# Performance work log

Hardware: AMD Instinct MI355X
Metric: run time of the kernel (lower is better)

The kernel has to match this reference:

```python
import jax, jax.numpy as jnp
import numpy as np

N, E, F_IN, D, H = 20000, 640000, 128, 16, 8  # nodes, edges, in_features, out_features, n_heads


def _linear_params(k, fan_in, fan_out):
    W = jax.random.normal(k, (fan_in, fan_out), jnp.float32) / np.sqrt(fan_in)
    b = jnp.zeros((fan_out,), jnp.float32)
    return W, b


def setup_inputs() -> dict:
    key = jax.random.key(0)
    ks = jax.random.split(key, 8)
    x = jax.random.normal(ks[0], (N, F_IN), jnp.float32)
    edge_index = jax.random.randint(ks[1], (2, E), 0, N, dtype=jnp.int64)
    Wq, bq = _linear_params(ks[2], F_IN, D * H)
    Wk, bk = _linear_params(ks[3], F_IN, D * H)
    Wv, bv = _linear_params(ks[4], F_IN, D * H)
    Wpsi, bpsi = _linear_params(ks[5], D, D)
    Wo, bo = _linear_params(ks[6], D * H * 2, F_IN)
    gamma = jnp.ones((F_IN,), jnp.float32)
    beta = jnp.zeros((F_IN,), jnp.float32)
    return {"x": x, "edge_index": edge_index, "Wq": Wq, "bq": bq, "Wk": Wk, "bk": bk,
            "Wv": Wv, "bv": bv, "Wpsi": Wpsi, "bpsi": bpsi, "Wo": Wo, "bo": bo,
            "gamma": gamma, "beta": beta}


def _segment_softmax(logits, seg, num_segments):
    # numerically-stable softmax of edge logits grouped by destination node (row)
    m = jax.ops.segment_max(logits, seg, num_segments=num_segments)  # [N,H]
    m = jnp.where(jnp.isfinite(m), m, 0.0)
    e = jnp.exp(logits - m[seg])  # [E,H]
    s = jax.ops.segment_sum(e, seg, num_segments=num_segments)  # [N,H]
    return e / (s[seg] + 1e-16)


def reference(x, edge_index, Wq, bq, Wk, bk, Wv, bv, Wpsi, bpsi, Wo, bo, gamma, beta):
    q = (x @ Wq + bq).reshape(N, H, D)
    k = (x @ Wk + bk).reshape(N, H, D)
    v = (x @ Wv + bv).reshape(N, H, D)
    row, col = edge_index[0], edge_index[1]

    logits = jnp.einsum('ehd,ehd->eh', q[row], k[col]) / np.sqrt(D)  # [E,H]
    alpha = _segment_softmax(logits, row, N)  # [E,H]

    v_j = v[col]  # [E,H,D]
    h_lp = jax.ops.segment_sum((alpha[..., None] * v_j).reshape(E, H * D), row, num_segments=N)
    v_bp = jnp.tanh(v_j @ Wpsi + bpsi)  # per-head linear on last dim, [E,H,D]
    h_bp = jax.ops.segment_sum((alpha[..., None] * v_bp).reshape(E, H * D), row, num_segments=N)

    h_out = jnp.concatenate([h_lp, h_bp], axis=1) @ Wo + bo  # [N,F_IN]
    y = x + jax.nn.relu(h_out)
    mu = jnp.mean(y, axis=-1, keepdims=True)
    var = jnp.mean(jnp.square(y - mu), axis=-1, keepdims=True)
    return (y - mu) * jax.lax.rsqrt(var + 1e-5) * gamma + beta
```

## Files before the change

### kernel.cpp

```cpp
#include <hip/hip_runtime.h>
#include <hip/hip_bf16.h>
#include <math.h>

#define NN 20000
#define EE 640000

typedef __attribute__((ext_vector_type(8))) short short8;
typedef __attribute__((ext_vector_type(4))) float f32x4;
typedef __hip_bfloat16 bf16;

__device__ inline ushort f2bf(float f) {
  bf16 h = __float2bfloat16(f);
  return *(ushort*)&h;
}
__device__ inline float bflo(uint u) { return __uint_as_float(u << 16); }
__device__ inline float bfhi(uint u) { return __uint_as_float(u & 0xFFFF0000u); }

__global__ __launch_bounds__(256) void prep_kernel(
    const float* __restrict__ x,
    const float* __restrict__ Wq, const float* __restrict__ Wk,
    const float* __restrict__ Wv, const float* __restrict__ Wo,
    const float* __restrict__ Wpsi, const float* __restrict__ bpsi,
    const float* __restrict__ bv,
    ushort* __restrict__ xb, ushort* __restrict__ Wts ,
    ushort* __restrict__ Wot, float* __restrict__ bvpsi) {
  __shared__ float T[128][129];
  __shared__ float WpsiS[256];
  __shared__ float bpsiS[16];
  int b = blockIdx.x, t = threadIdx.x;

  if (b < 1250) {
    int idx = b * 2048 + t * 8;
    const float* src = x + idx;
    float4 f0 = *(const float4*)(src);
    float4 f1 = *(const float4*)(src + 4);
    ushort tmp[8] = {f2bf(f0.x), f2bf(f0.y), f2bf(f0.z), f2bf(f0.w),
                     f2bf(f1.x), f2bf(f1.y), f2bf(f1.z), f2bf(f1.w)};
    *(uint4*)(xb + idx) = *(uint4*)tmp;
    return;
  }

  if (b <= 1254) {
    int which = b - 1250;
    const float* W;
    int k0 = 0;
    if (which < 3) W = (which == 0) ? Wq : (which == 1 ? Wk : Wv);
    else { W = Wo; k0 = (which - 3) * 128; }
    {
      int r = t >> 1, c0 = (t & 1) * 64;
      const float* src = W + (size_t)(k0 + r) * 128 + c0;
#pragma unroll
      for (int j = 0; j < 16; ++j) {
        float4 f = *(const float4*)(src + 4 * j);
        T[r][c0 + 4 * j + 0] = f.x; T[r][c0 + 4 * j + 1] = f.y;
        T[r][c0 + 4 * j + 2] = f.z; T[r][c0 + 4 * j + 3] = f.w;
      }
    }
    __syncthreads();
    int n = t >> 1, kh = (t & 1) * 64;
    if (which < 3) {
      ushort* dst = Wts + which * 16384 + n * 128 + kh;
#pragma unroll
      for (int j8 = 0; j8 < 8; ++j8) {
        ushort buf[8];
#pragma unroll
        for (int j = 0; j < 8; ++j) buf[j] = f2bf(T[kh + j8 * 8 + j][n]);
        *(uint4*)(dst + j8 * 8) = *(uint4*)buf;
      }
    } else {
      ushort* dst = Wot + n * 256 + k0 + kh;
#pragma unroll
      for (int j8 = 0; j8 < 8; ++j8) {
        ushort buf[8];
#pragma unroll
        for (int j = 0; j < 8; ++j) buf[j] = f2bf(T[kh + j8 * 8 + j][n]);
        *(uint4*)(dst + j8 * 8) = *(uint4*)buf;
      }
    }
    return;
  }

  {
    int r = t >> 1, c0 = (t & 1) * 64;
    const float* src = Wv + (size_t)r * 128 + c0;
#pragma unroll
    for (int j = 0; j < 16; ++j) {
      float4 f = *(const float4*)(src + 4 * j);
      T[r][c0 + 4 * j + 0] = f.x; T[r][c0 + 4 * j + 1] = f.y;
      T[r][c0 + 4 * j + 2] = f.z; T[r][c0 + 4 * j + 3] = f.w;
    }
    WpsiS[t] = Wpsi[t];
    if (t < 16) bpsiS[t] = bpsi[t];
  }
  __syncthreads();
  {
    int n = t >> 1, kh = (t & 1) * 64;
    int h = n >> 4, d = n & 15;
    ushort* dst = Wts + 3 * 16384 + n * 128 + kh;
    for (int k = 0; k < 64; ++k) {
      float acc = 0.f;
#pragma unroll
      for (int dp = 0; dp < 16; ++dp)
        acc = fmaf(T[kh + k][h * 16 + dp], WpsiS[dp * 16 + d], acc);
      dst[k] = f2bf(acc);
    }
    if (t < 128) {
      int hh = t >> 4, dd = t & 15;
      float acc = bpsiS[dd];
#pragma unroll
      for (int dp = 0; dp < 16; ++dp)
        acc = fmaf(bv[hh * 16 + dp], WpsiS[dp * 16 + dd], acc);
      bvpsi[t] = acc;
    }
  }
}

__global__ __launch_bounds__(256) void qkv_mfma(
    const ushort* __restrict__ xb, const ushort* __restrict__ Wts,
    const float* __restrict__ bq, const float* __restrict__ bk,
    const float* __restrict__ bv, const float* __restrict__ bvpsi,
    float* __restrict__ qbuf, ushort* __restrict__ kvb) {
  int t = threadIdx.x;
  int w = t >> 6, lane = t & 63;
  int m = lane & 15, qd = lane >> 4;
  int n0 = blockIdx.x * 128;
  int mat = blockIdx.y;
  const ushort* Wt = Wts + mat * 16384;
  const float* bias = (mat == 0) ? bq : (mat == 1 ? bk : (mat == 2 ? bv : bvpsi));
  int gr0 = n0 + w * 32;

  f32x4 acc0[8], acc1[8];
#pragma unroll
  for (int c = 0; c < 8; ++c) {
    acc0[c] = (f32x4){0.f, 0.f, 0.f, 0.f};
    acc1[c] = (f32x4){0.f, 0.f, 0.f, 0.f};
  }
#pragma unroll
  for (int kb = 0; kb < 4; ++kb) {
    int ko = kb * 32 + qd * 8;
    short8 a0 = *(const short8*)(xb + (size_t)(gr0 + m) * 128 + ko);
    short8 a1 = *(const short8*)(xb + (size_t)(gr0 + 16 + m) * 128 + ko);
#pragma unroll
    for (int c = 0; c < 8; ++c) {
      short8 bfr = *(const short8*)(Wt + (size_t)(c * 16 + m) * 128 + ko);
      acc0[c] = __builtin_amdgcn_mfma_f32_16x16x32_bf16(a0, bfr, acc0[c], 0, 0, 0);
      acc1[c] = __builtin_amdgcn_mfma_f32_16x16x32_bf16(a1, bfr, acc1[c], 0, 0, 0);
    }
  }
#pragma unroll
  for (int c = 0; c < 8; ++c) {
    int col = c * 16 + m;
    float bb = bias[col];
#pragma unroll
    for (int reg = 0; reg < 4; ++reg) {
      int row0 = gr0 + 4 * qd + reg;
      int row1 = row0 + 16;
      float v0 = acc0[c][reg] + bb;
      float v1 = acc1[c][reg] + bb;
      if (mat == 0) {
        if (row0 < NN) qbuf[(size_t)row0 * 128 + col] = v0;
        if (row1 < NN) qbuf[(size_t)row1 * 128 + col] = v1;
      } else if (mat < 3) {
        int off = (mat == 1) ? 0 : 128;
        if (row0 < NN) kvb[(size_t)row0 * 384 + off + col] = f2bf(v0);
        if (row1 < NN) kvb[(size_t)row1 * 384 + off + col] = f2bf(v1);
      } else {
        if (row0 < NN) kvb[(size_t)row0 * 384 + 256 + col] = f2bf(tanhf(v0));
        if (row1 < NN) kvb[(size_t)row1 * 384 + 256 + col] = f2bf(tanhf(v1));
      }
    }
  }
}

__global__ __launch_bounds__(256) void scatter_pad(const int* __restrict__ ei,
                                                   int* __restrict__ cursor,
                                                   int* __restrict__ scol) {
  int e = blockIdx.x * 256 + threadIdx.x;
  if (e < EE) {
    int r = ei[e];
    int c = ei[EE + e];
    int pos = atomicAdd(&cursor[r], 1);
    if (pos < 128) scol[r * 128 + pos] = c;
  }
}

__global__ __launch_bounds__(256) void aggregate_kernel(
    const float* __restrict__ qbuf, const ushort* __restrict__ kvb,
    const int* __restrict__ cursor, const int* __restrict__ scol,
    ushort* __restrict__ hb) {
  int wid = threadIdx.x >> 6, lane = threadIdx.x & 63;
  int node = blockIdx.x * 4 + wid;
  int e = lane >> 3, h = lane & 7;
  const float SC = 0.25f * 1.44269504f;

  float qv[16];
  {
    const float* qp = qbuf + (size_t)node * 128 + h * 16;
#pragma unroll
    for (int j = 0; j < 4; ++j) {
      float4 f = *(const float4*)(qp + 4 * j);
      qv[4 * j + 0] = f.x * SC; qv[4 * j + 1] = f.y * SC;
      qv[4 * j + 2] = f.z * SC; qv[4 * j + 3] = f.w * SC;
    }
  }
  int cnt = cursor[node];
  cnt = cnt > 128 ? 128 : cnt;
  int base = node * 128;

  float s = 0.f;
  float accV[16], accB[16];
#pragma unroll
  for (int j = 0; j < 16; ++j) { accV[j] = 0.f; accB[j] = 0.f; }

  for (int i0 = 0; i0 < cnt; i0 += 8) {
    int idx = i0 + e;
    bool valid = idx < cnt;
    int col = scol[base + (valid ? idx : 0)];
    const ushort* B = kvb + (size_t)col * 384 + h * 16;
    uint4 ka = *(const uint4*)(B);
    uint4 kb4 = *(const uint4*)(B + 8);
    uint4 va = *(const uint4*)(B + 128);
    uint4 vb4 = *(const uint4*)(B + 136);
    uint4 ta = *(const uint4*)(B + 256);
    uint4 tb4 = *(const uint4*)(B + 264);
    uint kk[8] = {ka.x, ka.y, ka.z, ka.w, kb4.x, kb4.y, kb4.z, kb4.w};
    uint vv[8] = {va.x, va.y, va.z, va.w, vb4.x, vb4.y, vb4.z, vb4.w};
    uint tt[8] = {ta.x, ta.y, ta.z, ta.w, tb4.x, tb4.y, tb4.z, tb4.w};
    float d = 0.f;
#pragma unroll
    for (int i = 0; i < 8; ++i) {
      d = fmaf(qv[2 * i], bflo(kk[i]), d);
      d = fmaf(qv[2 * i + 1], bfhi(kk[i]), d);
    }
    float wgt = valid ? exp2f(d) : 0.f;
    s += wgt;
#pragma unroll
    for (int i = 0; i < 8; ++i) {
      accV[2 * i]     = fmaf(wgt, bflo(vv[i]), accV[2 * i]);
      accV[2 * i + 1] = fmaf(wgt, bfhi(vv[i]), accV[2 * i + 1]);
      accB[2 * i]     = fmaf(wgt, bflo(tt[i]), accB[2 * i]);
      accB[2 * i + 1] = fmaf(wgt, bfhi(tt[i]), accB[2 * i + 1]);
    }
  }

#pragma unroll
  for (int mask = 8; mask <= 32; mask <<= 1) {
    s += __shfl_xor(s, mask);
#pragma unroll
    for (int j = 0; j < 16; ++j) {
      accV[j] += __shfl_xor(accV[j], mask);
      accB[j] += __shfl_xor(accB[j], mask);
    }
  }
  float inv = s > 0.f ? 1.f / s : 0.f;
  int dg = 2 * e;
  ushort* hp = hb + (size_t)node * 256 + h * 16 + dg;
  uint uv = (uint)f2bf(accV[dg] * inv) | ((uint)f2bf(accV[dg + 1] * inv) << 16);
  uint ub = (uint)f2bf(accB[dg] * inv) | ((uint)f2bf(accB[dg + 1] * inv) << 16);
  *(uint*)(hp) = uv;
  *(uint*)(hp + 128) = ub;
}

__global__ __launch_bounds__(256) void output_mfma(
    const ushort* __restrict__ hb, const ushort* __restrict__ Wot,
    const float* __restrict__ x, const float* __restrict__ bo,
    const float* __restrict__ gamma, const float* __restrict__ beta,
    float* __restrict__ out) {
  int t = threadIdx.x;
  int w = t >> 6, lane = t & 63;
  int m = lane & 15, qd = lane >> 4;
  int n0 = blockIdx.x * 128;
  int gr0 = n0 + w * 32;

  f32x4 acc0[8], acc1[8];
#pragma unroll
  for (int c = 0; c < 8; ++c) {
    acc0[c] = (f32x4){0.f, 0.f, 0.f, 0.f};
    acc1[c] = (f32x4){0.f, 0.f, 0.f, 0.f};
  }
#pragma unroll
  for (int kb = 0; kb < 8; ++kb) {
    int ko = kb * 32 + qd * 8;
    short8 a0 = *(const short8*)(hb + (size_t)(gr0 + m) * 256 + ko);
    short8 a1 = *(const short8*)(hb + (size_t)(gr0 + 16 + m) * 256 + ko);
#pragma unroll
    for (int c = 0; c < 8; ++c) {
      short8 bfr = *(const short8*)(Wot + (size_t)(c * 16 + m) * 256 + ko);
      acc0[c] = __builtin_amdgcn_mfma_f32_16x16x32_bf16(a0, bfr, acc0[c], 0, 0, 0);
      acc1[c] = __builtin_amdgcn_mfma_f32_16x16x32_bf16(a1, bfr, acc1[c], 0, 0, 0);
    }
  }
#pragma unroll
  for (int half = 0; half < 2; ++half) {
#pragma unroll
    for (int reg = 0; reg < 4; ++reg) {
      int row = gr0 + half * 16 + 4 * qd + reg;
      bool valid = row < NN;
      float vals[8];
      float sum = 0.f;
#pragma unroll
      for (int c = 0; c < 8; ++c) {
        int col = c * 16 + m;
        float a = (half ? acc1[c][reg] : acc0[c][reg]) + bo[col];
        a = fmaxf(a, 0.f);
        float xv = valid ? x[(size_t)row * 128 + col] : 0.f;
        float v = a + xv;
        vals[c] = v;
        sum += v;
      }
      sum += __shfl_xor(sum, 1); sum += __shfl_xor(sum, 2);
      sum += __shfl_xor(sum, 4); sum += __shfl_xor(sum, 8);
      float mean = sum * (1.f / 128.f);
      float ssq = 0.f;
#pragma unroll
      for (int c = 0; c < 8; ++c) {
        float d = vals[c] - mean;
        ssq = fmaf(d, d, ssq);
      }
      ssq += __shfl_xor(ssq, 1); ssq += __shfl_xor(ssq, 2);
      ssq += __shfl_xor(ssq, 4); ssq += __shfl_xor(ssq, 8);
      float rstd = rsqrtf(ssq * (1.f / 128.f) + 1e-5f);
      if (valid) {
#pragma unroll
        for (int c = 0; c < 8; ++c) {
          int col = c * 16 + m;
          out[(size_t)row * 128 + col] =
              (vals[c] - mean) * rstd * gamma[col] + beta[col];
        }
      }
    }
  }
}

extern "C" void kernel_launch(void* const* d_in, const int* in_sizes, int n_in,
                              void* d_out, int out_size, void* d_ws, size_t ws_size,
                              hipStream_t stream) {
  const float* x     = (const float*)d_in[0];
  const int*   ei    = (const int*)d_in[1];
  const float* Wq    = (const float*)d_in[2];
  const float* bq    = (const float*)d_in[3];
  const float* Wk    = (const float*)d_in[4];
  const float* bk    = (const float*)d_in[5];
  const float* Wv    = (const float*)d_in[6];
  const float* bv    = (const float*)d_in[7];
  const float* Wpsi  = (const float*)d_in[8];
  const float* bpsi  = (const float*)d_in[9];
  const float* Wo    = (const float*)d_in[10];
  const float* bo    = (const float*)d_in[11];
  const float* gamma = (const float*)d_in[12];
  const float* beta  = (const float*)d_in[13];
  float* out = (float*)d_out;

  char* ws = (char*)d_ws;
  ushort* xb    = (ushort*)(ws);
  ushort* Wts   = (ushort*)(ws + 5145600);
  ushort* Wot   = (ushort*)(ws + 5276672);
  float*  bvpsi = (float*) (ws + 5342208);
  float*  qbuf  = (float*) (ws + 5342720);
  ushort* kvb   = (ushort*)(ws + 15582720);
  ushort* hb    = (ushort*)(ws + 30942720);
  int*    cursor= (int*)   (ws + 41232128);
  int*    scol  = (int*)   (ws + 41312256);

  hipMemsetAsync(cursor, 0, 80000, stream);

  prep_kernel<<<1256, 256, 0, stream>>>(x, Wq, Wk, Wv, Wo, Wpsi, bpsi, bv,
                                        xb, Wts, Wot, bvpsi);
  qkv_mfma<<<dim3(157, 4), 256, 0, stream>>>(xb, Wts, bq, bk, bv, bvpsi,
                                             qbuf, kvb);
  scatter_pad<<<2500, 256, 0, stream>>>(ei, cursor, scol);
  aggregate_kernel<<<5000, 256, 0, stream>>>(qbuf, kvb, cursor, scol, hb);
  output_mfma<<<157, 256, 0, stream>>>(hb, Wot, x, bo, gamma, beta, out);
}
```

Measured before the change: 247.1 us.

## Fuse scatter into prep, store Q as bf16 via LDS tiles, reshape aggregation

The edge scatter now runs inside the prep kernel, which removes one launch. Transposes use half-size shared tiles. The QKV GEMM stages its results in an LDS tile and writes them as coalesced 16-byte stores, and Q is now stored as bf16 instead of fp32. Aggregation gives each node two waves, each covering 4 heads and 16 edges at a time, and splits the final reduction between the V and B accumulators. The output GEMM uses smaller blocks to raise occupancy. Storing Q in bf16 loses some precision, and the many changes interact with each other.

After: 247.6 us. About the same (+0.2%).

```diff
diff --git a/kernel.cpp b/kernel.cpp
--- a/kernel.cpp
+++ b/kernel.cpp
@@ -16,102 +16,103 @@
 __device__ inline float bflo(uint u) { return __uint_as_float(u << 16); }
 __device__ inline float bfhi(uint u) { return __uint_as_float(u & 0xFFFF0000u); }
 
-__global__ __launch_bounds__(256) void prep_kernel(
-    const float* __restrict__ x,
+__global__ __launch_bounds__(256) void prep_scatter(
+    const float* __restrict__ x, const int* __restrict__ ei,
     const float* __restrict__ Wq, const float* __restrict__ Wk,
     const float* __restrict__ Wv, const float* __restrict__ Wo,
     const float* __restrict__ Wpsi, const float* __restrict__ bpsi,
     const float* __restrict__ bv,
-    ushort* __restrict__ xb, ushort* __restrict__ Wts ,
-    ushort* __restrict__ Wot, float* __restrict__ bvpsi) {
-  __shared__ float T[128][129];
+    ushort* __restrict__ xb, ushort* __restrict__ Wts,
+    ushort* __restrict__ Wot, float* __restrict__ bvpsi,
+    int* __restrict__ cursor, int* __restrict__ scol) {
+  __shared__ float T[128][65];
   __shared__ float WpsiS[256];
   __shared__ float bpsiS[16];
   int b = blockIdx.x, t = threadIdx.x;
 
-  if (b < 1250) {
-    int idx = b * 2048 + t * 8;
-    const float* src = x + idx;
-    float4 f0 = *(const float4*)(src);
-    float4 f1 = *(const float4*)(src + 4);
+  if (b < 2500) {
+    int e = b * 256 + t;
+    int r = ei[e];
+    int c = ei[EE + e];
+    int pos = atomicAdd(&cursor[r], 1);
+    if (pos < 128) scol[r * 128 + pos] = c;
+    return;
+  }
+  if (b < 3750) {
+    int idx = (b - 2500) * 2048 + t * 8;
+    float4 f0 = *(const float4*)(x + idx);
+    float4 f1 = *(const float4*)(x + idx + 4);
     ushort tmp[8] = {f2bf(f0.x), f2bf(f0.y), f2bf(f0.z), f2bf(f0.w),
                      f2bf(f1.x), f2bf(f1.y), f2bf(f1.z), f2bf(f1.w)};
     *(uint4*)(xb + idx) = *(uint4*)tmp;
     return;
   }
-
-  if (b <= 1254) {
-    int which = b - 1250;
+  if (b <= 3754) {
+    int which = b - 3750;
     const float* W;
-    int k0 = 0;
-    if (which < 3) W = (which == 0) ? Wq : (which == 1 ? Wk : Wv);
-    else { W = Wo; k0 = (which - 3) * 128; }
-    {
-      int r = t >> 1, c0 = (t & 1) * 64;
-      const float* src = W + (size_t)(k0 + r) * 128 + c0;
-#pragma unroll
-      for (int j = 0; j < 16; ++j) {
+    int k0 = 0, dstride;
+    ushort* dst;
+    if (which < 3) { W = (which == 0) ? Wq : (which == 1 ? Wk : Wv);
+                     dst = Wts + which * 16384; dstride = 128; }
+    else { W = Wo; k0 = (which - 3) * 128; dst = Wot; dstride = 256; }
+    for (int h2 = 0; h2 < 2; ++h2) {
+      int r = t >> 1, c0 = (t & 1) * 32;
+      const float* src = W + (size_t)(k0 + r) * 128 + h2 * 64 + c0;
+#pragma unroll
+      for (int j = 0; j < 8; ++j) {
         float4 f = *(const float4*)(src + 4 * j);
         T[r][c0 + 4 * j + 0] = f.x; T[r][c0 + 4 * j + 1] = f.y;
         T[r][c0 + 4 * j + 2] = f.z; T[r][c0 + 4 * j + 3] = f.w;
       }
-    }
-    __syncthreads();
-    int n = t >> 1, kh = (t & 1) * 64;
-    if (which < 3) {
-      ushort* dst = Wts + which * 16384 + n * 128 + kh;
-#pragma unroll
-      for (int j8 = 0; j8 < 8; ++j8) {
-        ushort buf[8];
-#pragma unroll
-        for (int j = 0; j < 8; ++j) buf[j] = f2bf(T[kh + j8 * 8 + j][n]);
-        *(uint4*)(dst + j8 * 8) = *(uint4*)buf;
-      }
-    } else {
-      ushort* dst = Wot + n * 256 + k0 + kh;
-#pragma unroll
-      for (int j8 = 0; j8 < 8; ++j8) {
-        ushort buf[8];
-#pragma unroll
-        for (int j = 0; j < 8; ++j) buf[j] = f2bf(T[kh + j8 * 8 + j][n]);
-        *(uint4*)(dst + j8 * 8) = *(uint4*)buf;
-      }
+      __syncthreads();
+      int nl = t >> 2, kc = (t & 3) * 32;
+      int n = h2 * 64 + nl;
+      ushort buf[32];
+#pragma unroll
+      for (int k = 0; k < 32; ++k) buf[k] = f2bf(T[kc + k][nl]);
+      ushort* dp = dst + (size_t)n * dstride + k0 + kc;
+#pragma unroll
+      for (int j = 0; j < 4; ++j) *(uint4*)(dp + 8 * j) = ((uint4*)buf)[j];
+      __syncthreads();
     }
     return;
   }
-
-  {
-    int r = t >> 1, c0 = (t & 1) * 64;
-    const float* src = Wv + (size_t)r * 128 + c0;
-#pragma unroll
-    for (int j = 0; j < 16; ++j) {
+  WpsiS[t] = Wpsi[t];
+  if (t < 16) bpsiS[t] = bpsi[t];
+  for (int h2 = 0; h2 < 2; ++h2) {
+    int r = t >> 1, c0 = (t & 1) * 32;
+    const float* src = Wv + (size_t)r * 128 + h2 * 64 + c0;
+#pragma unroll
+    for (int j = 0; j < 8; ++j) {
       float4 f = *(const float4*)(src + 4 * j);
       T[r][c0 + 4 * j + 0] = f.x; T[r][c0 + 4 * j + 1] = f.y;
       T[r][c0 + 4 * j + 2] = f.z; T[r][c0 + 4 * j + 3] = f.w;
     }
-    WpsiS[t] = Wpsi[t];
-    if (t < 16) bpsiS[t] = bpsi[t];
-  }
-  __syncthreads();
-  {
-    int n = t >> 1, kh = (t & 1) * 64;
-    int h = n >> 4, d = n & 15;
-    ushort* dst = Wts + 3 * 16384 + n * 128 + kh;
-    for (int k = 0; k < 64; ++k) {
+    __syncthreads();
+    int nl = t >> 2, kc = (t & 3) * 32;
+    int n = h2 * 64 + nl;
+    int hh = n >> 4, dd = n & 15;
+    int lcb = hh * 16 - h2 * 64;
+    ushort buf[32];
+    for (int k = 0; k < 32; ++k) {
       float acc = 0.f;
 #pragma unroll
       for (int dp = 0; dp < 16; ++dp)
-        acc = fmaf(T[kh + k][h * 16 + dp], WpsiS[dp * 16 + d], acc);
-      dst[k] = f2bf(acc);
-    }
-    if (t < 128) {
-      int hh = t >> 4, dd = t & 15;
-      float acc = bpsiS[dd];
-#pragma unroll
-      for (int dp = 0; dp < 16; ++dp)
-        acc = fmaf(bv[hh * 16 + dp], WpsiS[dp * 16 + dd], acc);
-      bvpsi[t] = acc;
-    }
+        acc = fmaf(T[kc + k][lcb + dp], WpsiS[dp * 16 + dd], acc);
+      buf[k] = f2bf(acc);
+    }
+    ushort* dp2 = Wts + 3 * 16384 + (size_t)n * 128 + kc;
+#pragma unroll
+    for (int j = 0; j < 4; ++j) *(uint4*)(dp2 + 8 * j) = ((uint4*)buf)[j];
+    __syncthreads();
+  }
+  if (t < 128) {
+    int hh = t >> 4, dd = t & 15;
+    float acc = bpsiS[dd];
+#pragma unroll
+    for (int dp = 0; dp < 16; ++dp)
+      acc = fmaf(bv[hh * 16 + dp], WpsiS[dp * 16 + dd], acc);
+    bvpsi[t] = acc;
   }
 }
 
@@ -119,7 +120,8 @@
     const ushort* __restrict__ xb, const ushort* __restrict__ Wts,
     const float* __restrict__ bq, const float* __restrict__ bk,
     const float* __restrict__ bv, const float* __restrict__ bvpsi,
-    float* __restrict__ qbuf, ushort* __restrict__ kvb) {
+    ushort* __restrict__ qb, ushort* __restrict__ kvb) {
+  __shared__ ushort Tile[128 * 136];
   int t = threadIdx.x;
   int w = t >> 6, lane = t & 63;
   int m = lane & 15, qd = lane >> 4;
@@ -153,54 +155,46 @@
     float bb = bias[col];
 #pragma unroll
     for (int reg = 0; reg < 4; ++reg) {
-      int row0 = gr0 + 4 * qd + reg;
-      int row1 = row0 + 16;
       float v0 = acc0[c][reg] + bb;
       float v1 = acc1[c][reg] + bb;
-      if (mat == 0) {
-        if (row0 < NN) qbuf[(size_t)row0 * 128 + col] = v0;
-        if (row1 < NN) qbuf[(size_t)row1 * 128 + col] = v1;
-      } else if (mat < 3) {
-        int off = (mat == 1) ? 0 : 128;
-        if (row0 < NN) kvb[(size_t)row0 * 384 + off + col] = f2bf(v0);
-        if (row1 < NN) kvb[(size_t)row1 * 384 + off + col] = f2bf(v1);
-      } else {
-        if (row0 < NN) kvb[(size_t)row0 * 384 + 256 + col] = f2bf(tanhf(v0));
-        if (row1 < NN) kvb[(size_t)row1 * 384 + 256 + col] = f2bf(tanhf(v1));
-      }
-    }
-  }
-}
-
-__global__ __launch_bounds__(256) void scatter_pad(const int* __restrict__ ei,
-                                                   int* __restrict__ cursor,
-                                                   int* __restrict__ scol) {
-  int e = blockIdx.x * 256 + threadIdx.x;
-  if (e < EE) {
-    int r = ei[e];
-    int c = ei[EE + e];
-    int pos = atomicAdd(&cursor[r], 1);
-    if (pos < 128) scol[r * 128 + pos] = c;
+      if (mat == 3) { v0 = tanhf(v0); v1 = tanhf(v1); }
+      Tile[(w * 32 + 4 * qd + reg) * 136 + col] = f2bf(v0);
+      Tile[(w * 32 + 16 + 4 * qd + reg) * 136 + col] = f2bf(v1);
+    }
+  }
+  __syncthreads();
+  int row = t >> 1, half = (t & 1) * 64;
+  int grow = n0 + row;
+  if (grow < NN) {
+    const ushort* srcl = &Tile[row * 136 + half];
+    ushort* dstg;
+    if (mat == 0) dstg = qb + (size_t)grow * 128 + half;
+    else dstg = kvb + (size_t)grow * 384 + (mat == 1 ? 0 : (mat == 2 ? 128 : 256)) + half;
+#pragma unroll
+    for (int j = 0; j < 8; ++j)
+      *(uint4*)(dstg + 8 * j) = *(const uint4*)(srcl + 8 * j);
   }
 }
 
 __global__ __launch_bounds__(256) void aggregate_kernel(
-    const float* __restrict__ qbuf, const ushort* __restrict__ kvb,
+    const ushort* __restrict__ qb, const ushort* __restrict__ kvb,
     const int* __restrict__ cursor, const int* __restrict__ scol,
     ushort* __restrict__ hb) {
   int wid = threadIdx.x >> 6, lane = threadIdx.x & 63;
-  int node = blockIdx.x * 4 + wid;
-  int e = lane >> 3, h = lane & 7;
+  int node = blockIdx.x * 2 + (wid >> 1);
+  int e = lane >> 2, h = (wid & 1) * 4 + (lane & 3);
   const float SC = 0.25f * 1.44269504f;
 
   float qv[16];
   {
-    const float* qp = qbuf + (size_t)node * 128 + h * 16;
-#pragma unroll
-    for (int j = 0; j < 4; ++j) {
-      float4 f = *(const float4*)(qp + 4 * j);
-      qv[4 * j + 0] = f.x * SC; qv[4 * j + 1] = f.y * SC;
-      qv[4 * j + 2] = f.z * SC; qv[4 * j + 3] = f.w * SC;
+    const ushort* qp = qb + (size_t)node * 128 + h * 16;
+    uint4 a = *(const uint4*)qp;
+    uint4 b = *(const uint4*)(qp + 8);
+    uint qq[8] = {a.x, a.y, a.z, a.w, b.x, b.y, b.z, b.w};
+#pragma unroll
+    for (int i = 0; i < 8; ++i) {
+      qv[2 * i] = bflo(qq[i]) * SC;
+      qv[2 * i + 1] = bfhi(qq[i]) * SC;
     }
   }
   int cnt = cursor[node];
@@ -212,7 +206,7 @@
 #pragma unroll
   for (int j = 0; j < 16; ++j) { accV[j] = 0.f; accB[j] = 0.f; }
 
-  for (int i0 = 0; i0 < cnt; i0 += 8) {
+  for (int i0 = 0; i0 < cnt; i0 += 16) {
     int idx = i0 + e;
     bool valid = idx < cnt;
     int col = scol[base + (valid ? idx : 0)];
@@ -243,25 +237,30 @@
     }
   }
 
-#pragma unroll
-  for (int mask = 8; mask <= 32; mask <<= 1) {
+  s += __shfl_xor(s, 32);
+#pragma unroll
+  for (int j = 0; j < 16; ++j) {
+    accV[j] += __shfl_xor(accV[j], 32);
+    accB[j] += __shfl_xor(accB[j], 32);
+  }
+  bool pickV = e < 8;
+  float sel[16];
+#pragma unroll
+  for (int j = 0; j < 16; ++j) sel[j] = pickV ? accV[j] : accB[j];
+#pragma unroll
+  for (int mask = 4; mask <= 16; mask <<= 1) {
     s += __shfl_xor(s, mask);
 #pragma unroll
-    for (int j = 0; j < 16; ++j) {
-      accV[j] += __shfl_xor(accV[j], mask);
-      accB[j] += __shfl_xor(accB[j], mask);
-    }
+    for (int j = 0; j < 16; ++j) sel[j] += __shfl_xor(sel[j], mask);
   }
   float inv = s > 0.f ? 1.f / s : 0.f;
-  int dg = 2 * e;
-  ushort* hp = hb + (size_t)node * 256 + h * 16 + dg;
-  uint uv = (uint)f2bf(accV[dg] * inv) | ((uint)f2bf(accV[dg + 1] * inv) << 16);
-  uint ub = (uint)f2bf(accB[dg] * inv) | ((uint)f2bf(accB[dg + 1] * inv) << 16);
-  *(uint*)(hp) = uv;
-  *(uint*)(hp + 128) = ub;
-}
-
-__global__ __launch_bounds__(256) void output_mfma(
+  int dg = pickV ? 2 * e : 2 * (e - 8);
+  ushort* hp = hb + (size_t)node * 256 + (pickV ? 0 : 128) + h * 16 + dg;
+  uint u = (uint)f2bf(sel[dg] * inv) | ((uint)f2bf(sel[dg + 1] * inv) << 16);
+  *(uint*)hp = u;
+}
+
+__global__ __launch_bounds__(128) void output_mfma(
     const ushort* __restrict__ hb, const ushort* __restrict__ Wot,
     const float* __restrict__ x, const float* __restrict__ bo,
     const float* __restrict__ gamma, const float* __restrict__ beta,
@@ -269,8 +268,7 @@
   int t = threadIdx.x;
   int w = t >> 6, lane = t & 63;
   int m = lane & 15, qd = lane >> 4;
-  int n0 = blockIdx.x * 128;
-  int gr0 = n0 + w * 32;
+  int gr0 = blockIdx.x * 64 + w * 32;
 
   f32x4 acc0[8], acc1[8];
 #pragma unroll
@@ -353,22 +351,20 @@
 
   char* ws = (char*)d_ws;
   ushort* xb    = (ushort*)(ws);
-  ushort* Wts   = (ushort*)(ws + 5145600);
-  ushort* Wot   = (ushort*)(ws + 5276672);
-  float*  bvpsi = (float*) (ws + 5342208);
-  float*  qbuf  = (float*) (ws + 5342720);
-  ushort* kvb   = (ushort*)(ws + 15582720);
-  ushort* hb    = (ushort*)(ws + 30942720);
-  int*    cursor= (int*)   (ws + 41232128);
-  int*    scol  = (int*)   (ws + 41312256);
+  ushort* qb    = (ushort*)(ws + 5144576);
+  ushort* Wts   = (ushort*)(ws + 10289152);
+  ushort* Wot   = (ushort*)(ws + 10420224);
+  float*  bvpsi = (float*) (ws + 10485760);
+  ushort* kvb   = (ushort*)(ws + 10486272);
+  ushort* hb    = (ushort*)(ws + 25846272);
+  int*    cursor= (int*)   (ws + 36135424);
+  int*    scol  = (int*)   (ws + 36215552);
 
   hipMemsetAsync(cursor, 0, 80000, stream);
 
-  prep_kernel<<<1256, 256, 0, stream>>>(x, Wq, Wk, Wv, Wo, Wpsi, bpsi, bv,
-                                        xb, Wts, Wot, bvpsi);
-  qkv_mfma<<<dim3(157, 4), 256, 0, stream>>>(xb, Wts, bq, bk, bv, bvpsi,
-                                             qbuf, kvb);
-  scatter_pad<<<2500, 256, 0, stream>>>(ei, cursor, scol);
-  aggregate_kernel<<<5000, 256, 0, stream>>>(qbuf, kvb, cursor, scol, hb);
-  output_mfma<<<157, 256, 0, stream>>>(hb, Wot, x, bo, gamma, beta, out);
-}
+  prep_scatter<<<3756, 256, 0, stream>>>(x, ei, Wq, Wk, Wv, Wo, Wpsi, bpsi, bv,
+                                         xb, Wts, Wot, bvpsi, cursor, scol);
+  qkv_mfma<<<dim3(157, 4), 256, 0, stream>>>(xb, Wts, bq, bk, bv, bvpsi, qb, kvb);
+  aggregate_kernel<<<10000, 256, 0, stream>>>(qb, kvb, cursor, scol, hb);
+  output_mfma<<<314, 128, 0, stream>>>(hb, Wot, x, bo, gamma, beta, out);
+}
```
